# Performance work log

Hardware: AMD Instinct MI355X
Metric: run time of the kernel (lower is better)

## Reference

```python
import jax, jax.numpy as jnp
import numpy as np

B, L, V, DIN, H = 256, 256, 2048, 128, 256   # trees, leaves/tree, vocab, in_dim, mem_dim
NODES = 2 * L - 1                            # perfect binary tree, level-by-level layout
LEVELS = int(np.log2(L)) + 1                 # 9 levels: 256,128,...,1 nodes


def setup_inputs() -> dict:
    key = jax.random.key(0)
    ks = jax.random.split(key, 32)
    w = lambda k, shape: jax.random.normal(k, shape, jnp.float32) * 0.05
    inp = {
        "input_ids": jax.random.randint(ks[0], (B, NODES), 0, V),
        "emb": w(ks[1], (V, DIN)),
        # iou projections (i,o,u concatenated -> 3H)
        "Wioux": w(ks[2], (DIN, 3 * H)), "bioux": jnp.zeros((3 * H,), jnp.float32),
        "Wiouh1": w(ks[3], (H, 3 * H)), "biouh1": jnp.zeros((3 * H,), jnp.float32),
        "Wiouh2": w(ks[4], (H, 3 * H)), "biouh2": jnp.zeros((3 * H,), jnp.float32),
        # forget gates
        "Wfx": w(ks[5], (DIN, H)), "bfx": jnp.zeros((H,), jnp.float32),
        "Wfh11": w(ks[6], (H, H)), "bfh11": jnp.zeros((H,), jnp.float32),
        "Wfh12": w(ks[7], (H, H)), "bfh12": jnp.zeros((H,), jnp.float32),
        "Wfh21": w(ks[8], (H, H)), "bfh21": jnp.zeros((H,), jnp.float32),
        "Wfh22": w(ks[9], (H, H)), "bfh22": jnp.zeros((H,), jnp.float32),
        # classifier head
        "Wl1": w(ks[10], (H, 100)), "bl1": jnp.zeros((100,), jnp.float32),
        "Wl2": w(ks[11], (100, 1)), "bl2": jnp.zeros((1,), jnp.float32),
    }
    return inp


def reference(input_ids, emb, Wioux, bioux, Wiouh1, biouh1, Wiouh2, biouh2,
              Wfx, bfx, Wfh11, bfh11, Wfh12, bfh12, Wfh21, bfh21, Wfh22, bfh22,
              Wl1, bl1, Wl2, bl2):
    emb = emb.at[0].set(0.0)                 # padding_idx=0
    xemb = emb[input_ids]                    # [B, NODES, DIN]

    def cell(x, h1, h2, c1, c2):
        iou = (x @ Wioux + bioux) + (h1 @ Wiouh1 + biouh1) + (h2 @ Wiouh2 + biouh2)
        i, o, u = jnp.split(iou, 3, axis=-1)
        i, o, u = jax.nn.sigmoid(i), jax.nn.sigmoid(o), jnp.tanh(u)
        fx = x @ Wfx + bfx
        f0 = jax.nn.sigmoid((h1 @ Wfh11 + bfh11) + (h2 @ Wfh12 + bfh12) + fx)
        f1 = jax.nn.sigmoid((h1 @ Wfh21 + bfh21) + (h2 @ Wfh22 + bfh22) + fx)
        c = i * u + f0 * c1 + f1 * c2
        h = o * jnp.tanh(c)
        return h, c

    # leaves: zero child states
    z = jnp.zeros((B, L, H), jnp.float32)
    h, c = cell(xemb[:, :L], z, z, z, z)     # [B, L, H]

    off, n = 0, L
    for _ in range(LEVELS - 1):              # fixed small structural loop (8 iters)
        off += n
        n //= 2
        x = xemb[:, off:off + n]             # [B, n, DIN]
        h, c = cell(x, h[:, 0::2], h[:, 1::2], c[:, 0::2], c[:, 1::2])

    root_h = h[:, 0]                         # [B, H]
    hid = root_h @ Wl1 + bl1                 # linear1
    pred = (jax.nn.relu(hid) @ Wl2 + bl2)[..., 0]   # [B], arithmetic head (no softmax)
    return pred
```

## Files before the change

### kernel.cpp

```cpp
#include <hip/hip_runtime.h>
#include <math.h>

#define B_ 256
#define L_ 256
#define V_ 2048
#define DIN_ 128
#define H_ 256
#define NODES_ 511

typedef _Float16 half8 __attribute__((ext_vector_type(8)));
typedef float f32x4 __attribute__((ext_vector_type(4)));

__device__ __forceinline__ float sigm(float x) { return 1.f / (1.f + __expf(-x)); }
__device__ __forceinline__ float tanh_f(float x) {
    float xc = fminf(fmaxf(x, -15.f), 15.f);
    float e = __expf(2.f * xc);
    return (e - 1.f) / (e + 1.f);
}
__device__ __forceinline__ void gload16(const void* g, void* l) {
    __builtin_amdgcn_global_load_lds((const __attribute__((address_space(1))) unsigned int*)g,
                                     (__attribute__((address_space(3))) unsigned int*)l, 16, 0, 0);
}
template<int N> __device__ __forceinline__ void vwaitN() {
    asm volatile("s_waitcnt vmcnt(%0)" :: "i"(N) : "memory");
}

__global__ void build_WT(_Float16* __restrict__ WT,
    const float* __restrict__ Wioux, const float* __restrict__ Wfx,
    const float* __restrict__ Wiouh1, const float* __restrict__ Wfh11, const float* __restrict__ Wfh21,
    const float* __restrict__ Wiouh2, const float* __restrict__ Wfh12, const float* __restrict__ Wfh22)
{
    int e = blockIdx.x * 256 + threadIdx.x;
    int nn = e / 640, k = e - nn * 640;
    int g = nn >> 8, t = nn & 255;
    float v;
    if (k < 128) {
        v = (g < 3) ? Wioux[k * 768 + nn] : Wfx[k * 256 + t];
    } else if (k < 384) {
        int kp = k - 128;
        v = (g < 3) ? Wiouh1[kp * 768 + nn] : ((g == 3) ? Wfh11[kp * 256 + t] : Wfh21[kp * 256 + t]);
    } else {
        int kp = k - 384;
        v = (g < 3) ? Wiouh2[kp * 768 + nn] : ((g == 3) ? Wfh12[kp * 256 + t] : Wfh22[kp * 256 + t]);
    }
    WT[e] = (_Float16)v;
}

__global__ __launch_bounds__(256) void build_table(float* __restrict__ tabP, const float* __restrict__ emb,
    const float* __restrict__ Wioux, const float* __restrict__ Wfx,
    const float* __restrict__ bioux, const float* __restrict__ biouh1, const float* __restrict__ biouh2,
    const float* __restrict__ bfx, const float* __restrict__ bfh11, const float* __restrict__ bfh12,
    const float* __restrict__ bfh21, const float* __restrict__ bfh22)
{
    __shared__ float As[64][33];
    __shared__ float Ws[32][65];
    const int tid = threadIdx.x, tx = tid & 15, ty = tid >> 4;
    const int i0 = blockIdx.x * 64, c0 = blockIdx.y * 64;
    const int g = c0 >> 8;
    float acc[4][4];
    #pragma unroll
    for (int i = 0; i < 4; ++i)
        #pragma unroll
        for (int j = 0; j < 4; ++j) acc[i][j] = 0.f;

    for (int k0 = 0; k0 < 128; k0 += 32) {
        #pragma unroll
        for (int it = 0; it < 2; ++it) {
            int f = tid + it * 256;
            int row = f >> 3, kk = (f & 7) * 4;
            int gr = i0 + row;
            float4 av = (gr == 0) ? make_float4(0.f, 0.f, 0.f, 0.f)
                                  : *(const float4*)(emb + (size_t)gr * 128 + k0 + kk);
            As[row][kk] = av.x; As[row][kk + 1] = av.y; As[row][kk + 2] = av.z; As[row][kk + 3] = av.w;
            int k = f >> 4, cc = (f & 15) * 4;
            int col = c0 + cc;
            float4 wv = (g < 3) ? *(const float4*)(Wioux + (size_t)(k0 + k) * 768 + col)
                                : *(const float4*)(Wfx + (size_t)(k0 + k) * 256 + (col & 255));
            Ws[k][cc] = wv.x; Ws[k][cc + 1] = wv.y; Ws[k][cc + 2] = wv.z; Ws[k][cc + 3] = wv.w;
        }
        __syncthreads();
        #pragma unroll 8
        for (int k = 0; k < 32; ++k) {
            float a[4], w[4];
            #pragma unroll
            for (int i = 0; i < 4; ++i) a[i] = As[ty * 4 + i][k];
            #pragma unroll
            for (int j = 0; j < 4; ++j) w[j] = Ws[k][tx * 4 + j];
            #pragma unroll
            for (int i = 0; i < 4; ++i)
                #pragma unroll
                for (int j = 0; j < 4; ++j) acc[i][j] = fmaf(a[i], w[j], acc[i][j]);
        }
        __syncthreads();
    }
    #pragma unroll
    for (int j = 0; j < 4; ++j) {
        int col = c0 + tx * 4 + j; int t = col & 255;
        int p = t >> 4, q = t & 15;
        float bs = (g < 3) ? (bioux[col] + biouh1[col] + biouh2[col])
                 : (g == 3) ? (bfx[t] + bfh11[t] + bfh12[t])
                            : (bfx[t] + bfh21[t] + bfh22[t]);
        #pragma unroll
        for (int i = 0; i < 4; ++i) {
            int id = i0 + ty * 4 + i;
            tabP[((size_t)(id * 16 + p) * 5 + g) * 16 + q] = acc[i][j] + bs;
        }
    }
}

__global__ void build_h0c0(const float* __restrict__ tabP, _Float16* __restrict__ H0h, float* __restrict__ H0c) {
    int id = blockIdx.x, t = threadIdx.x;
    int p = t >> 4, q = t & 15;
    const float* tp = tabP + ((size_t)(id * 16 + p) * 5) * 16 + q;
    float vi = sigm(tp[0]), vo = sigm(tp[16]), vu = tanh_f(tp[32]);
    float c = vi * vu;
    H0h[id * 256 + t] = (_Float16)(vo * tanh_f(c));
    H0c[id * 256 + t] = c;
}

__global__ __launch_bounds__(256, 2) void build_G(
    const _Float16* __restrict__ WT, const _Float16* __restrict__ H0h, float* __restrict__ Gp)
{
    __shared__ __align__(16) char Asm[3][256 * 64];
    __shared__ __align__(16) char Bsm[3][4096];
    const int tid = threadIdx.x, lane = tid & 63, wid = tid >> 6;
    const int l15 = lane & 15, lg = lane >> 4;
    const int rowB = blockIdx.x * 256;
    const int C0 = blockIdx.y * 64;
    const int part = (C0 >= 1280) ? 1 : 0;
    const int nn0 = C0 - part * 1280;
    const int gg = nn0 >> 8;
    const int pb = (nn0 & 255) >> 4;

    const unsigned segOff = (unsigned)((((lane & 3) ^ ((lane >> 3) & 3))) * 16);
    unsigned srcA[4];
    #pragma unroll
    for (int i = 0; i < 4; ++i) {
        int rl = (wid * 4 + i) * 16 + (lane >> 2);
        srcA[i] = (unsigned)(rowB + rl) * 512u + segOff;
    }
    unsigned bsrc;
    {
        int cc = tid >> 2, j = tid & 3;
        int np = C0 + cc;
        int nn = np - part * 1280;
        bsrc = (unsigned)((nn * 640 + 128 + part * 256 + ((j ^ ((cc >> 1) & 3)) * 8)) * 2);
    }
    const char* hPB = (const char*)H0h;
    const char* wPB = (const char*)WT;

    f32x4 acc[4][4];
    #pragma unroll
    for (int rt = 0; rt < 4; ++rt)
        #pragma unroll
        for (int ct = 0; ct < 4; ++ct) acc[rt][ct] = (f32x4)0.f;

    const int xw = (l15 >> 1) & 3;

    auto STAGE = [&](int st, int buf) {
        #pragma unroll
        for (int i = 0; i < 4; ++i)
            gload16(hPB + srcA[i] + (unsigned)st * 64u, &Asm[buf][(wid * 4 + i) * 1024 + lane * 16]);
        gload16(wPB + bsrc + (unsigned)st * 64u, &Bsm[buf][tid * 16]);
    };
    auto COMPUTE = [&](int buf) {
        half8 aF[4];
        #pragma unroll
        for (int rt = 0; rt < 4; ++rt)
            aF[rt] = *(const half8*)&Asm[buf][(wid * 64 + rt * 16 + l15) * 64 + ((lg ^ xw) * 16)];
        #pragma unroll
        for (int ct = 0; ct < 4; ++ct) {
            int cc = ct * 16 + l15;
            half8 bF = *(const half8*)&Bsm[buf][cc * 64 + ((lg ^ ((cc >> 1) & 3)) * 16)];
            #pragma unroll
            for (int rt = 0; rt < 4; ++rt)
                acc[rt][ct] = __builtin_amdgcn_mfma_f32_16x16x32_f16(aF[rt], bF, acc[rt][ct], 0, 0, 0);
        }
    };
    auto WAITB = [&](bool counted) {
        if (counted) vwaitN<5>(); else vwaitN<0>();
        __builtin_amdgcn_s_barrier();
        __builtin_amdgcn_sched_barrier(0);
    };

    STAGE(0, 0); STAGE(1, 1); WAITB(true);
    #pragma unroll
    for (int S = 0; S < 8; ++S) {
        if (S + 2 < 8) STAGE(S + 2, (S + 2) % 3);
        COMPUTE(S % 3);
        if (S < 7) WAITB(S + 2 < 8);
    }

    #pragma unroll
    for (int rt = 0; rt < 4; ++rt)
        #pragma unroll
        for (int ct = 0; ct < 4; ++ct)
            #pragma unroll
            for (int q = 0; q < 4; ++q) {
                int id = rowB + wid * 64 + rt * 16 + lg * 4 + q;
                Gp[(((size_t)(id * 2 + part) * 16 + pb + ct) * 5 + gg) * 16 + l15] = acc[rt][ct][q];
            }
}

__global__ __launch_bounds__(256) void lvl1_combine(
    const float* __restrict__ tabP, const float* __restrict__ Gp,
    const float* __restrict__ H0c, const int* __restrict__ ids,
    _Float16* __restrict__ h_out, float* __restrict__ c_out)
{
    const int tid = threadIdx.x;
    const int c32 = tid & 31, rq = tid >> 5;
    const int bid = blockIdx.x;
    const int xcd = bid & 7, rank = bid >> 3;
    const int p = xcd * 2 + (c32 >> 4);
    const int l15 = c32 & 15;
    const int col = p * 16 + l15;
    #pragma unroll 4
    for (int it = 0; it < 32; ++it) {
        int row = rank * 256 + it * 8 + rq;
        int b = row >> 7, j = row & 127;
        const int* idr = ids + b * NODES_;
        int idp = idr[256 + j];
        int idA = idr[2 * j];
        int idB = idr[2 * j + 1];
        const float* tp = tabP + ((size_t)(idp * 16 + p) * 5) * 16 + l15;
        const float* g1 = Gp + (((size_t)(idA * 2 + 0) * 16 + p) * 5) * 16 + l15;
        const float* g2 = Gp + (((size_t)(idB * 2 + 1) * 16 + p) * 5) * 16 + l15;
        float pre0 = tp[0]  + g1[0]  + g2[0];
        float pre1 = tp[16] + g1[16] + g2[16];
        float pre2 = tp[32] + g1[32] + g2[32];
        float pre3 = tp[48] + g1[48] + g2[48];
        float pre4 = tp[64] + g1[64] + g2[64];
        float c1 = H0c[idA * 256 + col], c2 = H0c[idB * 256 + col];
        float vi = sigm(pre0), vo = sigm(pre1), vu = tanh_f(pre2);
        float vf0 = sigm(pre3), vf1 = sigm(pre4);
        float c = vi * vu + vf0 * c1 + vf1 * c2;
        h_out[(size_t)row * 256 + col] = (_Float16)(vo * tanh_f(c));
        c_out[(size_t)row * 256 + col] = c;
    }
}

template<int RT>
__global__ __launch_bounds__(256, (RT >= 4 ? 2 : 4)) void cellK(
    const _Float16* __restrict__ WT, const float* __restrict__ tabP,
    const int* __restrict__ ids,
    const _Float16* __restrict__ h_prev, const float* __restrict__ c_prev,
    _Float16* __restrict__ h_out, float* __restrict__ c_out,
    int n, int ln, int off, int nx)
{
    constexpr int BM = RT * 64;
    __shared__ __align__(16) char Asm[3][BM * 64];
    __shared__ __align__(16) char Bsm[3][5120];
    const int tid = threadIdx.x, lane = tid & 63, wid = tid >> 6;
    const int l15 = lane & 15, lg = lane >> 4;

    int bid = blockIdx.x, x, y;
    if ((nx & 7) == 0) { int xcd = bid & 7, rank = bid >> 3; x = xcd * (nx >> 3) + (rank >> 4); y = rank & 15; }
    else { x = bid >> 4; y = bid & 15; }
    const int rowB = x * BM;
    const int t0 = y * 16;

    const unsigned segOff = (unsigned)((((lane & 3) ^ ((lane >> 3) & 3))) * 16);
    unsigned srcA[RT];
    #pragma unroll
    for (int i = 0; i < RT; ++i) {
        int rl = (wid * RT + i) * 16 + (lane >> 2);
        srcA[i] = (unsigned)(rowB + rl) * 1024u + segOff;
    }
    unsigned bsrc0, bsrc1 = 0;
    {
        int nr = tid >> 2, j = tid & 3;
        int ng = (nr >> 4) * 256 + t0 + (nr & 15);
        bsrc0 = (unsigned)((ng * 640 + 128 + ((j ^ ((nr >> 1) & 3)) * 8)) * 2);
        if (wid == 0) {
            int ng2 = 1024 + t0 + (tid >> 2);
            int seg2 = (tid & 3) ^ ((tid >> 3) & 3);
            bsrc1 = (unsigned)((ng2 * 640 + 128 + seg2 * 8) * 2);
        }
    }
    const char* hPB = (const char*)h_prev;
    const char* wPB = (const char*)WT;

    f32x4 acc[RT][5];
    #pragma unroll
    for (int rt = 0; rt < RT; ++rt)
        #pragma unroll
        for (int g = 0; g < 5; ++g) acc[rt][g] = (f32x4)0.f;

    const int xw = (l15 >> 1) & 3;

    auto STAGE = [&](int st, int buf) {
        #pragma unroll
        for (int i = 0; i < RT; ++i)
            gload16(hPB + srcA[i] + (unsigned)st * 64u, &Asm[buf][(wid * RT + i) * 1024 + lane * 16]);
        gload16(wPB + bsrc0 + (unsigned)st * 64u, &Bsm[buf][tid * 16]);
        if (wid == 0) gload16(wPB + bsrc1 + (unsigned)st * 64u, &Bsm[buf][4096 + tid * 16]);
    };
    auto COMPUTE = [&](int buf) {
        half8 aF[RT];
        #pragma unroll
        for (int rt = 0; rt < RT; ++rt)
            aF[rt] = *(const half8*)&Asm[buf][(wid * RT * 16 + rt * 16 + l15) * 64 + ((lg ^ xw) * 16)];
        #pragma unroll
        for (int g = 0; g < 5; ++g) {
            half8 bF = *(const half8*)&Bsm[buf][(g * 16 + l15) * 64 + ((lg ^ xw) * 16)];
            #pragma unroll
            for (int rt = 0; rt < RT; ++rt)
                acc[rt][g] = __builtin_amdgcn_mfma_f32_16x16x32_f16(aF[rt], bF, acc[rt][g], 0, 0, 0);
        }
    };
    auto WAITB = [&](bool counted) {
        if (counted) { if (wid == 0) vwaitN<RT + 2>(); else vwaitN<RT + 1>(); }
        else vwaitN<0>();
        __builtin_amdgcn_s_barrier();
        __builtin_amdgcn_sched_barrier(0);
    };

    STAGE(0, 0);
    STAGE(1, 1);
    WAITB(true);

    #pragma unroll
    for (int S = 0; S < 16; ++S) {
        if (S + 2 < 16) STAGE(S + 2, (S + 2) % 3);
        COMPUTE(S % 3);
        if (S < 15) WAITB(S + 2 < 16);
    }

    const int tcol = t0 + l15;
    #pragma unroll
    for (int rt = 0; rt < RT; ++rt) {
        #pragma unroll
        for (int q = 0; q < 4; ++q) {
            int row = rowB + wid * (RT * 16) + rt * 16 + lg * 4 + q;
            int b = row >> ln, j = row & (n - 1);
            int idp = ids[b * NODES_ + off + j];
            const float* tp = tabP + ((size_t)(idp * 16 + y) * 5) * 16 + l15;
            const float* cpp = c_prev + (size_t)row * 512 + tcol;
            float c1 = cpp[0], c2 = cpp[256];
            float vi  = sigm(acc[rt][0][q] + tp[0]);
            float vo  = sigm(acc[rt][1][q] + tp[16]);
            float vu  = tanh_f(acc[rt][2][q] + tp[32]);
            float vf0 = sigm(acc[rt][3][q] + tp[48]);
            float vf1 = sigm(acc[rt][4][q] + tp[64]);
            float c = vi * vu + vf0 * c1 + vf1 * c2;
            size_t ob = (size_t)row * 256 + tcol;
            h_out[ob] = (_Float16)(vo * tanh_f(c));
            c_out[ob] = c;
        }
    }
}

__global__ void head_kernel(const _Float16* __restrict__ hroot,
    const float* __restrict__ Wl1, const float* __restrict__ bl1,
    const float* __restrict__ Wl2, const float* __restrict__ bl2,
    float* __restrict__ out)
{
    __shared__ float hrow[H_];
    __shared__ float red[256];
    int b = blockIdx.x; int tid = threadIdx.x;
    hrow[tid] = (float)hroot[(size_t)b * H_ + tid];
    __syncthreads();
    float v = 0.f;
    if (tid < 100) {
        float s = bl1[tid];
        for (int k = 0; k < H_; ++k) s = fmaf(hrow[k], Wl1[k * 100 + tid], s);
        v = fmaxf(s, 0.f) * Wl2[tid];
    }
    red[tid] = v;
    __syncthreads();
    for (int s = 128; s > 0; s >>= 1) { if (tid < s) red[tid] += red[tid + s]; __syncthreads(); }
    if (tid == 0) out[b] = red[0] + bl2[0];
}

extern "C" void kernel_launch(void* const* d_in, const int* in_sizes, int n_in,
                              void* d_out, int out_size, void* d_ws, size_t ws_size,
                              hipStream_t stream) {
    const int*   ids    = (const int*)d_in[0];
    const float* emb    = (const float*)d_in[1];
    const float* Wioux  = (const float*)d_in[2];
    const float* bioux  = (const float*)d_in[3];
    const float* Wiouh1 = (const float*)d_in[4];
    const float* biouh1 = (const float*)d_in[5];
    const float* Wiouh2 = (const float*)d_in[6];
    const float* biouh2 = (const float*)d_in[7];
    const float* Wfx    = (const float*)d_in[8];
    const float* bfx    = (const float*)d_in[9];
    const float* Wfh11  = (const float*)d_in[10];
    const float* bfh11  = (const float*)d_in[11];
    const float* Wfh12  = (const float*)d_in[12];
    const float* bfh12  = (const float*)d_in[13];
    const float* Wfh21  = (const float*)d_in[14];
    const float* bfh21  = (const float*)d_in[15];
    const float* Wfh22  = (const float*)d_in[16];
    const float* bfh22  = (const float*)d_in[17];
    const float* Wl1    = (const float*)d_in[18];
    const float* bl1    = (const float*)d_in[19];
    const float* Wl2    = (const float*)d_in[20];
    const float* bl2    = (const float*)d_in[21];
    float* out = (float*)d_out;

    char* wsb = (char*)d_ws;
    _Float16* WT   = (_Float16*)(wsb);
    float*    tabP = (float*)(wsb + 2167808);
    _Float16* H0h  = (_Float16*)(wsb + 12653568);
    float*    H0c  = (float*)(wsb + 13702144);
    _Float16* hA   = (_Float16*)(wsb + 15799296);
    _Float16* hB   = (_Float16*)(wsb + 24187904);
    float*    cA   = (float*)(wsb + 40965120);
    float*    cB   = (float*)(wsb + 57742336);
    float*    Gp   = (float*)(wsb + 91296768);

    build_WT<<<dim3(3200), 256, 0, stream>>>(WT, Wioux, Wfx, Wiouh1, Wfh11, Wfh21, Wiouh2, Wfh12, Wfh22);
    build_table<<<dim3(32, 20), 256, 0, stream>>>(tabP, emb, Wioux, Wfx,
        bioux, biouh1, biouh2, bfx, bfh11, bfh12, bfh21, bfh22);
    build_h0c0<<<dim3(2048), 256, 0, stream>>>(tabP, H0h, H0c);
    build_G<<<dim3(8, 40), 256, 0, stream>>>(WT, H0h, Gp);

    lvl1_combine<<<dim3(1024), 256, 0, stream>>>(tabP, Gp, H0c, ids, hB, cB);

    _Float16 *hp = hB, *hn = hA;
    float    *cp = cB, *cn = cA;
    int off = 384, n = 64, ln = 6;
    for (int lvl = 2; lvl <= 8; ++lvl) {
        int M = B_ * n;
        if (M >= 2048) {
            int nx = M / 256;
            cellK<4><<<dim3(nx * 16), 256, 0, stream>>>(WT, tabP, ids, hp, cp, hn, cn, n, ln, off, nx);
        } else if (M >= 1024) {
            int nx = M / 128;
            cellK<2><<<dim3(nx * 16), 256, 0, stream>>>(WT, tabP, ids, hp, cp, hn, cn, n, ln, off, nx);
        } else {
            int nx = M / 64;
            cellK<1><<<dim3(nx * 16), 256, 0, stream>>>(WT, tabP, ids, hp, cp, hn, cn, n, ln, off, nx);
        }
        off += n; n >>= 1; --ln;
        _Float16* t1 = hp; hp = hn; hn = t1;
        float*    t2 = cp; cp = cn; cn = t2;
    }

    head_kernel<<<dim3(256), 256, 0, stream>>>(hp, Wl1, bl1, Wl2, bl2, out);
}
```

Measured before the change: 237.9 us.

## Widen cell kernel N-tile to 32 hidden columns per block

Each block of the per-level cell GEMM now covers 32 hidden columns (two 16-wide groups) instead of 16. The B-tile staged in LDS doubles and the MFMA accumulators per lane double, so the grid launches half as many blocks. Each A-fragment (child hidden state) is reused across twice as many MFMAs, which cuts repeated A loads from global memory. In exchange it raises register and LDS pressure, lowers the occupancy hint for small RT, and leaves fewer blocks for the small late levels.

```diff
diff --git a/kernel.cpp b/kernel.cpp
--- a/kernel.cpp
+++ b/kernel.cpp
@@ -240,7 +240,7 @@
 }
 
 template<int RT>
-__global__ __launch_bounds__(256, (RT >= 4 ? 2 : 4)) void cellK(
+__global__ __launch_bounds__(256, (RT >= 4 ? 2 : 3)) void cellL(
     const _Float16* __restrict__ WT, const float* __restrict__ tabP,
     const int* __restrict__ ids,
     const _Float16* __restrict__ h_prev, const float* __restrict__ c_prev,
@@ -249,15 +249,15 @@
 {
     constexpr int BM = RT * 64;
     __shared__ __align__(16) char Asm[3][BM * 64];
-    __shared__ __align__(16) char Bsm[3][5120];
+    __shared__ __align__(16) char Bsm[3][10240];
     const int tid = threadIdx.x, lane = tid & 63, wid = tid >> 6;
     const int l15 = lane & 15, lg = lane >> 4;
 
     int bid = blockIdx.x, x, y;
-    if ((nx & 7) == 0) { int xcd = bid & 7, rank = bid >> 3; x = xcd * (nx >> 3) + (rank >> 4); y = rank & 15; }
-    else { x = bid >> 4; y = bid & 15; }
+    if ((nx & 7) == 0) { int xcd = bid & 7, rank = bid >> 3; x = xcd * (nx >> 3) + (rank >> 3); y = rank & 7; }
+    else { x = bid >> 3; y = bid & 7; }
     const int rowB = x * BM;
-    const int t0 = y * 16;
+    const int t0 = y * 32;
 
     const unsigned segOff = (unsigned)((((lane & 3) ^ ((lane >> 3) & 3))) * 16);
     unsigned srcA[RT];
@@ -266,25 +266,23 @@
         int rl = (wid * RT + i) * 16 + (lane >> 2);
         srcA[i] = (unsigned)(rowB + rl) * 1024u + segOff;
     }
-    unsigned bsrc0, bsrc1 = 0;
-    {
-        int nr = tid >> 2, j = tid & 3;
-        int ng = (nr >> 4) * 256 + t0 + (nr & 15);
-        bsrc0 = (unsigned)((ng * 640 + 128 + ((j ^ ((nr >> 1) & 3)) * 8)) * 2);
-        if (wid == 0) {
-            int ng2 = 1024 + t0 + (tid >> 2);
-            int seg2 = (tid & 3) ^ ((tid >> 3) & 3);
-            bsrc1 = (unsigned)((ng2 * 640 + 128 + seg2 * 8) * 2);
-        }
+    unsigned bsrc[3];
+    #pragma unroll
+    for (int q = 0; q < 3; ++q) {
+        int f = tid + q * 256;
+        int nr = f >> 2, j = f & 3;
+        int g = nr >> 5, tl = nr & 31;
+        int gn = g * 256 + t0 + tl;
+        bsrc[q] = (unsigned)((gn * 640 + 128 + ((j ^ ((nr >> 1) & 3)) * 8)) * 2);
     }
     const char* hPB = (const char*)h_prev;
     const char* wPB = (const char*)WT;
 
-    f32x4 acc[RT][5];
+    f32x4 acc[RT][10];
     #pragma unroll
     for (int rt = 0; rt < RT; ++rt)
         #pragma unroll
-        for (int g = 0; g < 5; ++g) acc[rt][g] = (f32x4)0.f;
+        for (int c = 0; c < 10; ++c) acc[rt][c] = (f32x4)0.f;
 
     const int xw = (l15 >> 1) & 3;
 
@@ -292,8 +290,9 @@
         #pragma unroll
         for (int i = 0; i < RT; ++i)
             gload16(hPB + srcA[i] + (unsigned)st * 64u, &Asm[buf][(wid * RT + i) * 1024 + lane * 16]);
-        gload16(wPB + bsrc0 + (unsigned)st * 64u, &Bsm[buf][tid * 16]);
-        if (wid == 0) gload16(wPB + bsrc1 + (unsigned)st * 64u, &Bsm[buf][4096 + tid * 16]);
+        gload16(wPB + bsrc[0] + (unsigned)st * 64u, &Bsm[buf][(size_t)tid * 16]);
+        gload16(wPB + bsrc[1] + (unsigned)st * 64u, &Bsm[buf][(size_t)(256 + tid) * 16]);
+        if (tid < 128) gload16(wPB + bsrc[2] + (unsigned)st * 64u, &Bsm[buf][(size_t)(512 + tid) * 16]);
     };
     auto COMPUTE = [&](int buf) {
         half8 aF[RT];
@@ -301,15 +300,18 @@
         for (int rt = 0; rt < RT; ++rt)
             aF[rt] = *(const half8*)&Asm[buf][(wid * RT * 16 + rt * 16 + l15) * 64 + ((lg ^ xw) * 16)];
         #pragma unroll
-        for (int g = 0; g < 5; ++g) {
-            half8 bF = *(const half8*)&Bsm[buf][(g * 16 + l15) * 64 + ((lg ^ xw) * 16)];
-            #pragma unroll
-            for (int rt = 0; rt < RT; ++rt)
-                acc[rt][g] = __builtin_amdgcn_mfma_f32_16x16x32_f16(aF[rt], bF, acc[rt][g], 0, 0, 0);
-        }
+        for (int g = 0; g < 5; ++g)
+            #pragma unroll
+            for (int th = 0; th < 2; ++th) {
+                int nr = g * 32 + th * 16 + l15;
+                half8 bF = *(const half8*)&Bsm[buf][(size_t)nr * 64 + ((lg ^ ((nr >> 1) & 3)) * 16)];
+                #pragma unroll
+                for (int rt = 0; rt < RT; ++rt)
+                    acc[rt][g * 2 + th] = __builtin_amdgcn_mfma_f32_16x16x32_f16(aF[rt], bF, acc[rt][g * 2 + th], 0, 0, 0);
+            }
     };
     auto WAITB = [&](bool counted) {
-        if (counted) { if (wid == 0) vwaitN<RT + 2>(); else vwaitN<RT + 1>(); }
+        if (counted) { if (wid < 2) vwaitN<RT + 3>(); else vwaitN<RT + 2>(); }
         else vwaitN<0>();
         __builtin_amdgcn_s_barrier();
         __builtin_amdgcn_sched_barrier(0);
@@ -326,7 +328,6 @@
         if (S < 15) WAITB(S + 2 < 16);
     }
 
-    const int tcol = t0 + l15;
     #pragma unroll
     for (int rt = 0; rt < RT; ++rt) {
         #pragma unroll
@@ -334,18 +335,23 @@
             int row = rowB + wid * (RT * 16) + rt * 16 + lg * 4 + q;
             int b = row >> ln, j = row & (n - 1);
             int idp = ids[b * NODES_ + off + j];
-            const float* tp = tabP + ((size_t)(idp * 16 + y) * 5) * 16 + l15;
-            const float* cpp = c_prev + (size_t)row * 512 + tcol;
-            float c1 = cpp[0], c2 = cpp[256];
-            float vi  = sigm(acc[rt][0][q] + tp[0]);
-            float vo  = sigm(acc[rt][1][q] + tp[16]);
-            float vu  = tanh_f(acc[rt][2][q] + tp[32]);
-            float vf0 = sigm(acc[rt][3][q] + tp[48]);
-            float vf1 = sigm(acc[rt][4][q] + tp[64]);
-            float c = vi * vu + vf0 * c1 + vf1 * c2;
-            size_t ob = (size_t)row * 256 + tcol;
-            h_out[ob] = (_Float16)(vo * tanh_f(c));
-            c_out[ob] = c;
+            #pragma unroll
+            for (int th = 0; th < 2; ++th) {
+                int tcol = t0 + th * 16 + l15;
+                int p = y * 2 + th;
+                const float* tp = tabP + ((size_t)(idp * 16 + p) * 5) * 16 + l15;
+                const float* cpp = c_prev + (size_t)row * 512 + tcol;
+                float c1 = cpp[0], c2 = cpp[256];
+                float vi  = sigm(acc[rt][0 + th][q] + tp[0]);
+                float vo  = sigm(acc[rt][2 + th][q] + tp[16]);
+                float vu  = tanh_f(acc[rt][4 + th][q] + tp[32]);
+                float vf0 = sigm(acc[rt][6 + th][q] + tp[48]);
+                float vf1 = sigm(acc[rt][8 + th][q] + tp[64]);
+                float c = vi * vu + vf0 * c1 + vf1 * c2;
+                size_t ob = (size_t)row * 256 + tcol;
+                h_out[ob] = (_Float16)(vo * tanh_f(c));
+                c_out[ob] = c;
+            }
         }
     }
 }
@@ -425,13 +431,13 @@
         int M = B_ * n;
         if (M >= 2048) {
             int nx = M / 256;
-            cellK<4><<<dim3(nx * 16), 256, 0, stream>>>(WT, tabP, ids, hp, cp, hn, cn, n, ln, off, nx);
+            cellL<4><<<dim3(nx * 8), 256, 0, stream>>>(WT, tabP, ids, hp, cp, hn, cn, n, ln, off, nx);
         } else if (M >= 1024) {
             int nx = M / 128;
-            cellK<2><<<dim3(nx * 16), 256, 0, stream>>>(WT, tabP, ids, hp, cp, hn, cn, n, ln, off, nx);
+            cellL<2><<<dim3(nx * 8), 256, 0, stream>>>(WT, tabP, ids, hp, cp, hn, cn, n, ln, off, nx);
         } else {
             int nx = M / 64;
-            cellK<1><<<dim3(nx * 16), 256, 0, stream>>>(WT, tabP, ids, hp, cp, hn, cn, n, ln, off, nx);
+            cellL<1><<<dim3(nx * 8), 256, 0, stream>>>(WT, tabP, ids, hp, cp, hn, cn, n, ln, off, nx);
         }
         off += n; n >>= 1; --ln;
         _Float16* t1 = hp; hp = hn; hn = t1;
```

After: 343.2 us. 44.3% more time.
